# Kernel optimization log

Measured on AMD Instinct MI355X. Metric: run time of the kernel, lower is better.

## Reference

```python
import jax, jax.numpy as jnp
import numpy as np

QMAX = 127.0

def _sym_quantize(t):
    # per-tensor symmetric int8 fake-quant: returns (quantized values as float, scale)
    scale = jnp.max(jnp.abs(t)) / QMAX
    q = jnp.clip(jnp.round(t / scale), -QMAX, QMAX)
    return q, scale

def setup_inputs() -> dict:
    key = jax.random.key(0)
    k1, k2, k3 = jax.random.split(key, 3)
    TOKENS, IN_F, OUT_F = 4096, 4096, 4096
    x = jax.random.normal(k1, (TOKENS, IN_F), dtype=jnp.float32)
    # int8-valued weight buffer (stored int32 for portability), symmetric range
    quantized_weight = jax.random.randint(k2, (OUT_F, IN_F), -127, 128, dtype=jnp.int32)
    weight_scale = jnp.float32(0.01)  # scalar per-tensor weight scale buffer
    bias = jax.random.normal(k3, (OUT_F,), dtype=jnp.float32)
    return {"x": x, "quantized_weight": quantized_weight,
            "weight_scale": weight_scale, "bias": bias}

def reference(x, quantized_weight, weight_scale, bias):
    q_x, x_scale = _sym_quantize(x)                      # [T, In] fake-quant activations
    w = quantized_weight.astype(jnp.float32)             # [Out, In]
    out = jnp.matmul(q_x, w.T)                           # fp32 GEMM on int8-valued operands
    out = out * (x_scale * weight_scale)                 # dequant scaling
    out = out + bias
    return out
```

## Files before the change

kernel.cpp:

```cpp
#include <hip/hip_runtime.h>

typedef __attribute__((ext_vector_type(4))) int int4v;

#define NB_MAX 1024

__device__ __forceinline__ void async_ld16(const void* g, void* l) {
  __builtin_amdgcn_global_load_lds(
      (const __attribute__((address_space(1))) void*)g,
      (__attribute__((address_space(3))) void*)l,
      16, 0, 0);
}

__global__ void absmax_wpack_kernel(const float* __restrict__ x,
                                    const int* __restrict__ w,
                                    float* __restrict__ partial,
                                    int* __restrict__ qw, int n4, int nw4) {
  const float4* x4 = (const float4*)x;
  float m = 0.0f;
  const int stride = gridDim.x * blockDim.x;
  const int i0 = blockIdx.x * blockDim.x + threadIdx.x;
  for (int i = i0; i < n4; i += stride) {
    float4 v = x4[i];
    m = fmaxf(m, fabsf(v.x));
    m = fmaxf(m, fabsf(v.y));
    m = fmaxf(m, fabsf(v.z));
    m = fmaxf(m, fabsf(v.w));
  }
  for (int i = i0; i < nw4; i += stride) {
    int4 v = ((const int4*)w)[i];
    unsigned int p = (unsigned int)(v.x & 255) |
                     ((unsigned int)(v.y & 255) << 8) |
                     ((unsigned int)(v.z & 255) << 16) |
                     ((unsigned int)(v.w & 255) << 24);
    qw[i] = (int)p;
  }
#pragma unroll
  for (int off = 32; off > 0; off >>= 1)
    m = fmaxf(m, __shfl_down(m, off, 64));
  __shared__ float wmax[4];
  const int wid = threadIdx.x >> 6;
  if ((threadIdx.x & 63) == 0) wmax[wid] = m;
  __syncthreads();
  if (threadIdx.x == 0)
    partial[blockIdx.x] =
        fmaxf(fmaxf(wmax[0], wmax[1]), fmaxf(wmax[2], wmax[3]));
}

__device__ __forceinline__ float reduce_partials(const float* partial) {
  __shared__ float smax;
  float m = 0.0f;
  for (int i = threadIdx.x; i < NB_MAX; i += blockDim.x)
    m = fmaxf(m, partial[i]);
#pragma unroll
  for (int off = 32; off > 0; off >>= 1)
    m = fmaxf(m, __shfl_down(m, off, 64));
  __shared__ float wmax[4];
  const int wid = threadIdx.x >> 6;
  if ((threadIdx.x & 63) == 0) wmax[wid] = m;
  __syncthreads();
  if (threadIdx.x == 0)
    smax = fmaxf(fmaxf(wmax[0], wmax[1]), fmaxf(wmax[2], wmax[3]));
  __syncthreads();
  return smax;
}

__global__ void quant_x_kernel(const float* __restrict__ x,
                               const float* __restrict__ partial,
                               float* __restrict__ scale_slot,
                               int* __restrict__ qx, int nx4) {
  const float scale = reduce_partials(partial) / 127.0f;
  if (blockIdx.x == 0 && threadIdx.x == 0) *scale_slot = scale;
  const int stride = gridDim.x * blockDim.x;
  for (int i = blockIdx.x * blockDim.x + threadIdx.x; i < nx4; i += stride) {
    float4 v = ((const float4*)x)[i];
    int q0 = (int)fminf(fmaxf(rintf(v.x / scale), -127.0f), 127.0f);
    int q1 = (int)fminf(fmaxf(rintf(v.y / scale), -127.0f), 127.0f);
    int q2 = (int)fminf(fmaxf(rintf(v.z / scale), -127.0f), 127.0f);
    int q3 = (int)fminf(fmaxf(rintf(v.w / scale), -127.0f), 127.0f);
    unsigned int p = (unsigned int)(q0 & 255) |
                     ((unsigned int)(q1 & 255) << 8) |
                     ((unsigned int)(q2 & 255) << 16) |
                     ((unsigned int)(q3 & 255) << 24);
    qx[i] = (int)p;
  }
}

__global__ __launch_bounds__(512, 2) void gemm_i8_kernel(
    const signed char* __restrict__ A,
    const signed char* __restrict__ B,
    const float* __restrict__ bias,
    const float* __restrict__ scale_slot,
    const float* __restrict__ wscale,
    float* __restrict__ out, int K, int N) {
  __shared__ signed char As[2][256 * 128];
  __shared__ signed char Bs[2][256 * 128];

  const int tid = threadIdx.x;
  const int lane = tid & 63;
  const int wid = tid >> 6;

  const int nwgx = gridDim.x;
  const int nwg = nwgx * gridDim.y;
  const int flat = blockIdx.y * nwgx + blockIdx.x;
  const int cpx = nwg >> 3;
  const int swz = (flat & 7) * cpx + (flat >> 3);
  const int row0 = (swz / nwgx) << 8;
  const int col0 = (swz % nwgx) << 8;

  const int wm = (wid >> 2) * 128;
  const int wn = (wid & 3) * 64;

  int4v acc[8][4] = {};

  const int srow = wid * 8 + (lane >> 3);
  const int schunk = ((lane & 7) ^ ((lane >> 3) & 7)) << 4;
  const signed char* gA = A + (long)(row0 + srow) * K + schunk;
  const signed char* gB = B + (long)(col0 + srow) * K + schunk;
  const int sdst = wid * 1024;

  const int q = lane >> 4;
  const int c7 = lane & 7;
  const int fc0 = (q ^ c7) << 4;
  const int fc1 = ((4 + q) ^ c7) << 4;
  const int fa = (wm + (lane & 15)) * 128;
  const int fb = (wn + (lane & 15)) * 128;

  const long l64K = 64 * (long)K;
  const int NT = K >> 7;

  async_ld16(gB, &Bs[0][0 * 8192 + sdst]);
  async_ld16(gB + l64K, &Bs[0][1 * 8192 + sdst]);
  async_ld16(gB + 2 * l64K, &Bs[0][2 * 8192 + sdst]);
  async_ld16(gB + 3 * l64K, &Bs[0][3 * 8192 + sdst]);
  async_ld16(gA, &As[0][0 * 8192 + sdst]);
  async_ld16(gA + 2 * l64K, &As[0][2 * 8192 + sdst]);
  async_ld16(gA + l64K, &As[0][1 * 8192 + sdst]);
  async_ld16(gA + 3 * l64K, &As[0][3 * 8192 + sdst]);
  asm volatile("s_waitcnt vmcnt(2)" ::: "memory");
  __builtin_amdgcn_s_barrier();

  int4v areg[4][2], breg0[2][2], breg1[2][2];

  for (int T = 0; T < NT; ++T) {
    const int b = T & 1;
    const bool pf = (T + 1 < NT);
    const signed char* gAn = gA + (long)(T + 1) * 128;
    const signed char* gBn = gB + (long)(T + 1) * 128;
    signed char* An = &As[b ^ 1][sdst];
    signed char* Bn = &Bs[b ^ 1][sdst];
    const signed char* Ab = As[b];
    const signed char* Bb = Bs[b];

#pragma unroll
    for (int i = 0; i < 4; i++) {
      areg[i][0] = *(const int4v*)(Ab + fa + i * 2048 + fc0);
      areg[i][1] = *(const int4v*)(Ab + fa + i * 2048 + fc1);
    }
#pragma unroll
    for (int j = 0; j < 2; j++) {
      breg0[j][0] = *(const int4v*)(Bb + fb + j * 2048 + fc0);
      breg0[j][1] = *(const int4v*)(Bb + fb + j * 2048 + fc1);
    }
    if (pf) {
      async_ld16(gBn, Bn);
      async_ld16(gBn + l64K, Bn + 8192);
      async_ld16(gBn + 2 * l64K, Bn + 2 * 8192);
      async_ld16(gBn + 3 * l64K, Bn + 3 * 8192);
    }
    __builtin_amdgcn_s_barrier();
    asm volatile("s_waitcnt lgkmcnt(0)" ::: "memory");
    __builtin_amdgcn_s_setprio(1);
#pragma unroll
    for (int i = 0; i < 4; i++)
#pragma unroll
      for (int j = 0; j < 2; j++) {
        acc[i][j] = __builtin_amdgcn_mfma_i32_16x16x64_i8(areg[i][0], breg0[j][0], acc[i][j], 0, 0, 0);
        acc[i][j] = __builtin_amdgcn_mfma_i32_16x16x64_i8(areg[i][1], breg0[j][1], acc[i][j], 0, 0, 0);
      }
    __builtin_amdgcn_s_setprio(0);
    __builtin_amdgcn_s_barrier();

#pragma unroll
    for (int j = 0; j < 2; j++) {
      breg1[j][0] = *(const int4v*)(Bb + fb + (2 + j) * 2048 + fc0);
      breg1[j][1] = *(const int4v*)(Bb + fb + (2 + j) * 2048 + fc1);
    }
    if (pf) {
      async_ld16(gAn, An);
      async_ld16(gAn + 2 * l64K, An + 2 * 8192);
      async_ld16(gAn + l64K, An + 8192);
      async_ld16(gAn + 3 * l64K, An + 3 * 8192);
    }
    __builtin_amdgcn_s_barrier();
    asm volatile("s_waitcnt lgkmcnt(0)" ::: "memory");
    __builtin_amdgcn_s_setprio(1);
#pragma unroll
    for (int i = 0; i < 4; i++)
#pragma unroll
      for (int j = 0; j < 2; j++) {
        acc[i][2 + j] = __builtin_amdgcn_mfma_i32_16x16x64_i8(areg[i][0], breg1[j][0], acc[i][2 + j], 0, 0, 0);
        acc[i][2 + j] = __builtin_amdgcn_mfma_i32_16x16x64_i8(areg[i][1], breg1[j][1], acc[i][2 + j], 0, 0, 0);
      }
    __builtin_amdgcn_s_setprio(0);
    if (pf) {
      asm volatile("s_waitcnt vmcnt(8)" ::: "memory");
    } else {
      asm volatile("s_waitcnt vmcnt(0)" ::: "memory");
    }
    __builtin_amdgcn_s_barrier();

#pragma unroll
    for (int i = 0; i < 4; i++) {
      areg[i][0] = *(const int4v*)(Ab + fa + 8192 + i * 2048 + fc0);
      areg[i][1] = *(const int4v*)(Ab + fa + 8192 + i * 2048 + fc1);
    }
    __builtin_amdgcn_s_barrier();
    asm volatile("s_waitcnt lgkmcnt(0)" ::: "memory");
    __builtin_amdgcn_s_setprio(1);
#pragma unroll
    for (int i = 0; i < 4; i++)
#pragma unroll
      for (int j = 0; j < 2; j++) {
        acc[4 + i][j] = __builtin_amdgcn_mfma_i32_16x16x64_i8(areg[i][0], breg0[j][0], acc[4 + i][j], 0, 0, 0);
        acc[4 + i][j] = __builtin_amdgcn_mfma_i32_16x16x64_i8(areg[i][1], breg0[j][1], acc[4 + i][j], 0, 0, 0);
      }
    __builtin_amdgcn_s_setprio(0);
    __builtin_amdgcn_s_barrier();

    __builtin_amdgcn_s_barrier();
    __builtin_amdgcn_s_setprio(1);
#pragma unroll
    for (int i = 0; i < 4; i++)
#pragma unroll
      for (int j = 0; j < 2; j++) {
        acc[4 + i][2 + j] = __builtin_amdgcn_mfma_i32_16x16x64_i8(areg[i][0], breg1[j][0], acc[4 + i][2 + j], 0, 0, 0);
        acc[4 + i][2 + j] = __builtin_amdgcn_mfma_i32_16x16x64_i8(areg[i][1], breg1[j][1], acc[4 + i][2 + j], 0, 0, 0);
      }
    __builtin_amdgcn_s_setprio(0);
    asm volatile("s_waitcnt vmcnt(2)" ::: "memory");
    __builtin_amdgcn_s_barrier();
  }

  asm volatile("s_waitcnt vmcnt(0)" ::: "memory");
  __syncthreads();

  float* lds = (float*)&As[0][0];
  const float s = scale_slot[0] * wscale[0];
  const int l15 = lane & 15;
  float bv[4];
#pragma unroll
  for (int jj = 0; jj < 4; jj++) bv[jj] = bias[col0 + wn + l15 + jj * 16];
  const int wbase = wid << 11;
#pragma unroll
  for (int g = 0; g < 8; ++g) {
    float* reg = lds + wbase + ((g & 1) << 10);
#pragma unroll
    for (int jj = 0; jj < 4; jj++)
#pragma unroll
      for (int r = 0; r < 4; r++)
        reg[(q * 4 + r) * 64 + l15 + jj * 16] = (float)acc[g][jj][r] * s + bv[jj];
    asm volatile("s_waitcnt lgkmcnt(0)" ::: "memory");
    __builtin_amdgcn_sched_barrier(0);
#pragma unroll
    for (int rr = 0; rr < 4; rr++) {
      const int row = q + rr * 4;
      float4 v = *(const float4*)(reg + row * 64 + l15 * 4);
      *(float4*)(out + (long)(row0 + wm + g * 16 + row) * N + col0 + wn +
                 l15 * 4) = v;
    }
  }
}

extern "C" void kernel_launch(void* const* d_in, const int* in_sizes, int n_in,
                              void* d_out, int out_size, void* d_ws,
                              size_t ws_size, hipStream_t stream) {
  const float* x = (const float*)d_in[0];
  const int* w = (const int*)d_in[1];
  const float* wscale = (const float*)d_in[2];
  const float* bias = (const float*)d_in[3];
  float* out = (float*)d_out;

  const int OUT_F = in_sizes[3];
  const int IN_F = in_sizes[1] / OUT_F;
  const int TOKENS = in_sizes[0] / IN_F;

  float* partial = (float*)d_ws;
  float* scale_slot = partial + NB_MAX;
  signed char* qx = (signed char*)d_ws + 8192;
  signed char* qw = qx + (size_t)TOKENS * IN_F;

  const int nx4 = TOKENS * IN_F / 4;
  const int nw4 = OUT_F * IN_F / 4;

  absmax_wpack_kernel<<<NB_MAX, 256, 0, stream>>>(x, w, partial, (int*)qw,
                                                  nx4, nw4);

  quant_x_kernel<<<2048, 256, 0, stream>>>(x, partial, scale_slot, (int*)qx,
                                           nx4);

  dim3 grid(OUT_F / 256, TOKENS / 256);
  gemm_i8_kernel<<<grid, 512, 0, stream>>>(qx, qw, bias, scale_slot, wscale,
                                           out, IN_F, OUT_F);
}
```

Measured before the change: 244.6 us.

## Fuse absmax and quantize into one kernel with grid barrier; direct epilogue stores

Merges the absmax/weight-pack and activation-quantize kernels into a single persistent kernel that uses an atomic counter as a grid-wide barrier. Weight packing runs between the partial-max write and the barrier to hide the wait, and one kernel launch is removed. The x reads in the quantize pass may now hit cache because the same blocks read the same data. The GEMM epilogue drops the LDS transpose and writes scalar floats straight to global memory, which gives less coalesced stores. The grid barrier depends on all 1024 blocks being resident at the same time.

```diff
diff --git a/kernel.cpp b/kernel.cpp
--- a/kernel.cpp
+++ b/kernel.cpp
@@ -2,7 +2,7 @@
 
 typedef __attribute__((ext_vector_type(4))) int int4v;
 
-#define NB_MAX 1024
+#define PREP_GRID 1024
 
 __device__ __forceinline__ void async_ld16(const void* g, void* l) {
   __builtin_amdgcn_global_load_lds(
@@ -11,21 +11,34 @@
       16, 0, 0);
 }
 
-__global__ void absmax_wpack_kernel(const float* __restrict__ x,
-                                    const int* __restrict__ w,
-                                    float* __restrict__ partial,
-                                    int* __restrict__ qw, int n4, int nw4) {
-  const float4* x4 = (const float4*)x;
-  float m = 0.0f;
+__global__ __launch_bounds__(256, 4) void prep_kernel(
+    const float* __restrict__ x, const int* __restrict__ w,
+    float* __restrict__ partial, unsigned int* __restrict__ counter,
+    float* __restrict__ scale_slot, int* __restrict__ qx,
+    int* __restrict__ qw, int nx4, int nw4) {
   const int stride = gridDim.x * blockDim.x;
   const int i0 = blockIdx.x * blockDim.x + threadIdx.x;
-  for (int i = i0; i < n4; i += stride) {
-    float4 v = x4[i];
+  __shared__ float wmax[4];
+  __shared__ float smax;
+
+  float m = 0.0f;
+  for (int i = i0; i < nx4; i += stride) {
+    float4 v = ((const float4*)x)[i];
     m = fmaxf(m, fabsf(v.x));
     m = fmaxf(m, fabsf(v.y));
     m = fmaxf(m, fabsf(v.z));
     m = fmaxf(m, fabsf(v.w));
   }
+#pragma unroll
+  for (int off = 32; off > 0; off >>= 1)
+    m = fmaxf(m, __shfl_down(m, off, 64));
+  const int wv = threadIdx.x >> 6;
+  if ((threadIdx.x & 63) == 0) wmax[wv] = m;
+  __syncthreads();
+  if (threadIdx.x == 0)
+    partial[blockIdx.x] =
+        fmaxf(fmaxf(wmax[0], wmax[1]), fmaxf(wmax[2], wmax[3]));
+
   for (int i = i0; i < nw4; i += stride) {
     int4 v = ((const int4*)w)[i];
     unsigned int p = (unsigned int)(v.x & 255) |
@@ -34,44 +47,33 @@
                      ((unsigned int)(v.w & 255) << 24);
     qw[i] = (int)p;
   }
+
+  __syncthreads();
+  if (threadIdx.x == 0) {
+    __threadfence();
+    __hip_atomic_fetch_add(counter, 1u, __ATOMIC_ACQ_REL,
+                           __HIP_MEMORY_SCOPE_AGENT);
+    while (__hip_atomic_load(counter, __ATOMIC_ACQUIRE,
+                             __HIP_MEMORY_SCOPE_AGENT) < gridDim.x)
+      __builtin_amdgcn_s_sleep(2);
+  }
+  __syncthreads();
+
+  float mm = 0.0f;
+  for (int i = threadIdx.x; i < (int)gridDim.x; i += blockDim.x)
+    mm = fmaxf(mm, partial[i]);
 #pragma unroll
   for (int off = 32; off > 0; off >>= 1)
-    m = fmaxf(m, __shfl_down(m, off, 64));
-  __shared__ float wmax[4];
-  const int wid = threadIdx.x >> 6;
-  if ((threadIdx.x & 63) == 0) wmax[wid] = m;
-  __syncthreads();
-  if (threadIdx.x == 0)
-    partial[blockIdx.x] =
-        fmaxf(fmaxf(wmax[0], wmax[1]), fmaxf(wmax[2], wmax[3]));
-}
-
-__device__ __forceinline__ float reduce_partials(const float* partial) {
-  __shared__ float smax;
-  float m = 0.0f;
-  for (int i = threadIdx.x; i < NB_MAX; i += blockDim.x)
-    m = fmaxf(m, partial[i]);
-#pragma unroll
-  for (int off = 32; off > 0; off >>= 1)
-    m = fmaxf(m, __shfl_down(m, off, 64));
-  __shared__ float wmax[4];
-  const int wid = threadIdx.x >> 6;
-  if ((threadIdx.x & 63) == 0) wmax[wid] = m;
+    mm = fmaxf(mm, __shfl_down(mm, off, 64));
+  if ((threadIdx.x & 63) == 0) wmax[wv] = mm;
   __syncthreads();
   if (threadIdx.x == 0)
     smax = fmaxf(fmaxf(wmax[0], wmax[1]), fmaxf(wmax[2], wmax[3]));
   __syncthreads();
-  return smax;
-}
-
-__global__ void quant_x_kernel(const float* __restrict__ x,
-                               const float* __restrict__ partial,
-                               float* __restrict__ scale_slot,
-                               int* __restrict__ qx, int nx4) {
-  const float scale = reduce_partials(partial) / 127.0f;
-  if (blockIdx.x == 0 && threadIdx.x == 0) *scale_slot = scale;
-  const int stride = gridDim.x * blockDim.x;
-  for (int i = blockIdx.x * blockDim.x + threadIdx.x; i < nx4; i += stride) {
+  const float scale = smax / 127.0f;
+  if (i0 == 0) *scale_slot = scale;
+
+  for (int i = i0; i < nx4; i += stride) {
     float4 v = ((const float4*)x)[i];
     int q0 = (int)fminf(fmaxf(rintf(v.x / scale), -127.0f), 127.0f);
     int q1 = (int)fminf(fmaxf(rintf(v.y / scale), -127.0f), 127.0f);
@@ -242,31 +244,20 @@
   }
 
   asm volatile("s_waitcnt vmcnt(0)" ::: "memory");
-  __syncthreads();
-
-  float* lds = (float*)&As[0][0];
+
   const float s = scale_slot[0] * wscale[0];
-  const int l15 = lane & 15;
-  float bv[4];
-#pragma unroll
-  for (int jj = 0; jj < 4; jj++) bv[jj] = bias[col0 + wn + l15 + jj * 16];
-  const int wbase = wid << 11;
-#pragma unroll
-  for (int g = 0; g < 8; ++g) {
-    float* reg = lds + wbase + ((g & 1) << 10);
-#pragma unroll
-    for (int jj = 0; jj < 4; jj++)
-#pragma unroll
-      for (int r = 0; r < 4; r++)
-        reg[(q * 4 + r) * 64 + l15 + jj * 16] = (float)acc[g][jj][r] * s + bv[jj];
-    asm volatile("s_waitcnt lgkmcnt(0)" ::: "memory");
-    __builtin_amdgcn_sched_barrier(0);
-#pragma unroll
-    for (int rr = 0; rr < 4; rr++) {
-      const int row = q + rr * 4;
-      float4 v = *(const float4*)(reg + row * 64 + l15 * 4);
-      *(float4*)(out + (long)(row0 + wm + g * 16 + row) * N + col0 + wn +
-                 l15 * 4) = v;
+  const int orow = row0 + wm + (q << 2);
+  const int ocol0 = col0 + wn + (lane & 15);
+#pragma unroll
+  for (int jj = 0; jj < 4; jj++) {
+    const int c = ocol0 + jj * 16;
+    const float bv = bias[c];
+#pragma unroll
+    for (int g = 0; g < 8; g++) {
+#pragma unroll
+      for (int r = 0; r < 4; r++) {
+        out[(long)(orow + g * 16 + r) * N + c] = (float)acc[g][jj][r] * s + bv;
+      }
     }
   }
 }
@@ -285,20 +276,21 @@
   const int TOKENS = in_sizes[0] / IN_F;
 
   float* partial = (float*)d_ws;
-  float* scale_slot = partial + NB_MAX;
-  signed char* qx = (signed char*)d_ws + 8192;
-  signed char* qw = qx + (size_t)TOKENS * IN_F;
+  float* scale_slot = (float*)((char*)d_ws + 4096);
+  unsigned int* counter = (unsigned int*)((char*)d_ws + 4352);
+  int* qx = (int*)((char*)d_ws + 16384);
+  int* qw = (int*)((char*)d_ws + 16384 + (size_t)TOKENS * IN_F);
 
   const int nx4 = TOKENS * IN_F / 4;
   const int nw4 = OUT_F * IN_F / 4;
 
-  absmax_wpack_kernel<<<NB_MAX, 256, 0, stream>>>(x, w, partial, (int*)qw,
-                                                  nx4, nw4);
-
-  quant_x_kernel<<<2048, 256, 0, stream>>>(x, partial, scale_slot, (int*)qx,
-                                           nx4);
+  hipMemsetAsync((void*)counter, 0, 4, stream);
+
+  prep_kernel<<<PREP_GRID, 256, 0, stream>>>(x, w, partial, counter,
+                                             scale_slot, qx, qw, nx4, nw4);
 
   dim3 grid(OUT_F / 256, TOKENS / 256);
-  gemm_i8_kernel<<<grid, 512, 0, stream>>>(qx, qw, bias, scale_slot, wscale,
-                                           out, IN_F, OUT_F);
-}
+  gemm_i8_kernel<<<grid, 512, 0, stream>>>(
+      (const signed char*)qx, (const signed char*)qw, bias, scale_slot, wscale,
+      out, IN_F, OUT_F);
+}
```

New measurement: 357.7 us. 46.2% more time.
